# Kernel tuning notes

Hardware: AMD Instinct MI355X
Metric: run time of the kernel (lower is better)

Reference implementation:

```python
import jax, jax.numpy as jnp
import numpy as np

EPS = 1e-5

def binarize(w):
    # sign() binarization with straight-through estimator (identity grad)
    s = jnp.where(w >= 0, 1.0, -1.0).astype(w.dtype)
    return w + jax.lax.stop_gradient(s - w)

def batchnorm(x, gamma, beta):
    # BatchNorm1d in training mode: biased batch statistics over axis 0
    mean = jnp.mean(x, axis=0)
    var = jnp.mean(jnp.square(x - mean), axis=0)
    return (x - mean) * jax.lax.rsqrt(var + EPS) * gamma + beta

def setup_inputs() -> dict:
    key = jax.random.key(0)
    ks = jax.random.split(key, 3)
    B, D_IN, D_H, D_OUT = 65536, 784, 300, 10
    x = jax.random.normal(ks[0], (B, D_IN), dtype=jnp.float32)
    W1 = jax.random.normal(ks[1], (D_H, D_IN), dtype=jnp.float32) * 0.05
    W2 = jax.random.normal(ks[2], (D_OUT, D_H), dtype=jnp.float32) * 0.05
    gamma1 = jnp.ones((D_H,), jnp.float32)
    beta1 = jnp.zeros((D_H,), jnp.float32)
    gamma2 = jnp.ones((D_OUT,), jnp.float32)
    beta2 = jnp.zeros((D_OUT,), jnp.float32)
    return {"x": x, "W1": W1, "gamma1": gamma1, "beta1": beta1,
            "W2": W2, "gamma2": gamma2, "beta2": beta2}

def reference(x, W1, gamma1, beta1, W2, gamma2, beta2):
    h = x @ binarize(W1).T            # [B, 300]
    h = batchnorm(h, gamma1, beta1)
    o = h @ binarize(W2).T            # [B, 10]
    return batchnorm(o, gamma2, beta2)
```

## Files before the change

### kernel.cpp

```cpp
#include <hip/hip_runtime.h>
#include <cstdint>
#include <cstddef>

#define B_ROWS 65536
#define D_IN   784
#define KP     800
#define D_H    300
#define NP     320
#define D_OUT  10
#define NP2    16
#define EPS    1e-5f
#define NBLK   1024
#define APAD   44

typedef _Float16 half8  __attribute__((ext_vector_type(8)));
typedef float    floatx4 __attribute__((ext_vector_type(4)));

#define OFF_S1   ((size_t)0)
#define OFF_H    ((size_t)512000)
#define OFF_ST1  (OFF_H + (size_t)41943040)
#define OFF_W2   (OFF_ST1 + (size_t)2560)
#define OFF_ST2  (OFF_W2 + (size_t)10240)
#define OFF_OC   (OFF_ST2 + (size_t)256)
#define OFF_P1   OFF_OC
#define OFF_P2   (OFF_OC + (size_t)4194304)

__global__ void k_prep1(const float* __restrict__ W1, _Float16* __restrict__ S1)
{
    int idx = blockIdx.x * 256 + threadIdx.x;
    int n = idx / KP;
    int k = idx - n * KP;
    float v = 0.0f;
    if (n < D_H && k < D_IN)
        v = (W1[n * D_IN + k] >= 0.0f) ? 1.0f : -1.0f;
    S1[idx] = (_Float16)v;
}


#define PF_B(BV, NK)                                                        \
    _Pragma("unroll")                                                       \
    for (int nt = 0; nt < 5; ++nt)                                          \
        BV[nt] = *(const half8*)(bb + (size_t)nt * 16 * KP + (NK));

#define STAGE_LOAD(KK)                                                      \
    {                                                                       \
        sv0 = (floatx4){}; sv1 = (floatx4){};                               \
        if ((KK) + sc < D_IN) {               \
            sv0 = *(const floatx4*)(sxp + (KK));                            \
            sv1 = *(const floatx4*)(sxp + (KK) + 4);                        \
        }                                                                   \
    }

#define STAGE_STORE(BUF)                                                    \
    {                                                                       \
        half8 hv;                                                           \
        _Pragma("unroll")                                                   \
        for (int i2 = 0; i2 < 4; ++i2) {                                    \
            hv[i2]     = (_Float16)sv0[i2];                                 \
            hv[4 + i2] = (_Float16)sv1[i2];                                 \
        }                                                                   \
        *(half8*)&Alds[BUF][srow][sc] = hv;                                 \
    }

#define AFRAG(BUF)                                                          \
    _Pragma("unroll")                                                       \
    for (int mt = 0; mt < 4; ++mt)                                          \
        a[mt] = *(const half8*)&Alds[BUF][mt * 16 + row15][quad * 8];

#define COMPUTE(BV)                                                         \
    _Pragma("unroll")                                                       \
    for (int nt = 0; nt < 5; ++nt)                                          \
        _Pragma("unroll")                                                   \
        for (int mt = 0; mt < 4; ++mt)                                      \
            acc[mt][nt] = __builtin_amdgcn_mfma_f32_16x16x32_f16(           \
                a[mt], BV[nt], acc[mt][nt], 0, 0, 0);

__global__ __launch_bounds__(256) void k_gemm1(const float* __restrict__ x,
                                               const _Float16* __restrict__ S1,
                                               _Float16* __restrict__ h,
                                               float* __restrict__ part)
{
    __shared__ _Float16 Alds[2][64][APAD];
    const int t     = threadIdx.x;
    const int wave  = t >> 6;
    const int lane  = t & 63;
    const int row15 = lane & 15;
    const int quad  = lane >> 4;
    const int m0    = blockIdx.x * 64;

    const int srow = t >> 2;
    const int sc   = (t & 3) * 8;
    const float* sxp = x + (size_t)(m0 + srow) * D_IN + sc;

    const _Float16* bb = S1 + (size_t)(wave * 80 + row15) * KP + quad * 8;

    floatx4 acc[4][5] = {};
    half8   b0[5], b1[5];
    half8   a[4];
    floatx4 sv0, sv1;

    STAGE_LOAD(0)
    STAGE_STORE(0)
    PF_B(b0, 0)
    __syncthreads();

    for (int i = 0; i < 12; ++i) {
        const int kk = i * 64;
        STAGE_LOAD(kk + 32)
        PF_B(b1, kk + 32)
        AFRAG(0)
        COMPUTE(b0)
        STAGE_STORE(1)
        __syncthreads();
        STAGE_LOAD(kk + 64)
        PF_B(b0, kk + 64)
        AFRAG(1)
        COMPUTE(b1)
        STAGE_STORE(0)
        __syncthreads();
    }
    AFRAG(0)
    COMPUTE(b0)

    float s[5] = {}, q[5] = {};
#pragma unroll
    for (int mt = 0; mt < 4; ++mt)
#pragma unroll
        for (int nt = 0; nt < 5; ++nt)
#pragma unroll
            for (int r = 0; r < 4; ++r) {
                float v = acc[mt][nt][r];
                int m = m0 + mt * 16 + quad * 4 + r;
                int n = wave * 80 + nt * 16 + row15;
                h[(size_t)m * NP + n] = (_Float16)v;
                s[nt] += v;
                q[nt] += v * v;
            }
#pragma unroll
    for (int nt = 0; nt < 5; ++nt) {
        s[nt] += __shfl_xor(s[nt], 16); s[nt] += __shfl_xor(s[nt], 32);
        q[nt] += __shfl_xor(q[nt], 16); q[nt] += __shfl_xor(q[nt], 32);
    }
    if (quad == 0) {
#pragma unroll
        for (int nt = 0; nt < 5; ++nt) {
            int col = wave * 80 + nt * 16 + row15;
            part[(size_t)col * NBLK + blockIdx.x]        = s[nt];
            part[(size_t)(NP + col) * NBLK + blockIdx.x] = q[nt];
        }
    }
}

__global__ void k_stat1(const float* __restrict__ part, const float* __restrict__ gamma1,
                        const float* __restrict__ W2, _Float16* __restrict__ w2h)
{
    __shared__ float redS[4], redQ[4];
    const int j = blockIdx.x;
    const int t = threadIdx.x;
    const float* ps = part + (size_t)j * NBLK;
    const float* pq = part + (size_t)(NP + j) * NBLK;
    float s = ps[t] + ps[t + 256] + ps[t + 512] + ps[t + 768];
    float q = pq[t] + pq[t + 256] + pq[t + 512] + pq[t + 768];
#pragma unroll
    for (int off = 1; off < 64; off <<= 1) {
        s += __shfl_xor(s, off);
        q += __shfl_xor(q, off);
    }
    if ((t & 63) == 0) { redS[t >> 6] = s; redQ[t >> 6] = q; }
    __syncthreads();
    if (t < NP2) {
        float S = redS[0] + redS[1] + redS[2] + redS[3];
        float Q = redQ[0] + redQ[1] + redQ[2] + redQ[3];
        float mean = S * (1.0f / 65536.0f);
        float var  = Q * (1.0f / 65536.0f) - mean * mean;
        float a1   = 0.0f;
        if (j < D_H) a1 = gamma1[j] / sqrtf(var + EPS);
        float w = 0.0f;
        if (t < D_OUT && j < D_H)
            w = (W2[t * D_H + j] >= 0.0f) ? a1 : -a1;
        w2h[t * NP + j] = (_Float16)w;
    }
}

__global__ __launch_bounds__(256) void k_gemm2(const _Float16* __restrict__ h,
                                               const _Float16* __restrict__ w2h,
                                               float* __restrict__ oc,
                                               float* __restrict__ part2)
{
    __shared__ _Float16 Wlds[16][328];
    __shared__ float reds[4][16], redq[4][16];
    const int t     = threadIdx.x;
    const int wave  = t >> 6;
    const int lane  = t & 63;
    const int row15 = lane & 15;
    const int quad  = lane >> 4;

    for (int c = t; c < 640; c += 256) {
        int r  = c / 40;
        int cc = (c - r * 40) * 8;
        *(half8*)&Wlds[r][cc] = *(const half8*)(w2h + r * NP + cc);
    }
    __syncthreads();

    const int m0 = blockIdx.x * 64 + wave * 16;
    const _Float16* hp = h + (size_t)(m0 + row15) * NP + quad * 8;
    floatx4 acc = {};
#pragma unroll
    for (int kk = 0; kk < NP; kk += 32) {
        half8 a2 = *(const half8*)(hp + kk);
        half8 b2 = *(const half8*)&Wlds[row15][kk + quad * 8];
        acc = __builtin_amdgcn_mfma_f32_16x16x32_f16(a2, b2, acc, 0, 0, 0);
    }
    float s = 0.f, q = 0.f;
#pragma unroll
    for (int r = 0; r < 4; ++r) {
        float v = acc[r];
        oc[(size_t)(m0 + quad * 4 + r) * NP2 + row15] = v;
        s += v; q += v * v;
    }
    s += __shfl_xor(s, 16); s += __shfl_xor(s, 32);
    q += __shfl_xor(q, 16); q += __shfl_xor(q, 32);
    if (lane < 16) { reds[wave][row15] = s; redq[wave][row15] = q; }
    __syncthreads();
    if (t < 16) {
        float S = reds[0][t] + reds[1][t] + reds[2][t] + reds[3][t];
        float Q = redq[0][t] + redq[1][t] + redq[2][t] + redq[3][t];
        part2[(size_t)t * NBLK + blockIdx.x]          = S;
        part2[(size_t)(16 + t) * NBLK + blockIdx.x]   = Q;
    }
}

__global__ void k_stat2(const float* __restrict__ part2, const float* __restrict__ gamma2,
                        float* __restrict__ st2)
{
    __shared__ float redS[4], redQ[4];
    const int k = blockIdx.x;
    const int t = threadIdx.x;
    const float* ps = part2 + (size_t)k * NBLK;
    const float* pq = part2 + (size_t)(16 + k) * NBLK;
    float s = ps[t] + ps[t + 256] + ps[t + 512] + ps[t + 768];
    float q = pq[t] + pq[t + 256] + pq[t + 512] + pq[t + 768];
#pragma unroll
    for (int off = 1; off < 64; off <<= 1) {
        s += __shfl_xor(s, off);
        q += __shfl_xor(q, off);
    }
    if ((t & 63) == 0) { redS[t >> 6] = s; redQ[t >> 6] = q; }
    __syncthreads();
    if (t == 0) {
        float S = redS[0] + redS[1] + redS[2] + redS[3];
        float Q = redQ[0] + redQ[1] + redQ[2] + redQ[3];
        float mean = S * (1.0f / 65536.0f);
        float var  = Q * (1.0f / 65536.0f) - mean * mean;
        float sc   = (k < D_OUT) ? gamma2[k] / sqrtf(var + EPS) : 0.0f;
        st2[k]      = mean;
        st2[16 + k] = sc;
    }
}

__global__ void k_final(const float* __restrict__ oc, const float* __restrict__ st2,
                        const float* __restrict__ beta2, float* __restrict__ out)
{
    int idx = blockIdx.x * 256 + threadIdx.x;
    int m = idx / 10;
    int k = idx - m * 10;
    float mean = st2[k];
    float sc   = st2[16 + k];
    out[idx] = (oc[(size_t)m * NP2 + k] - mean) * sc + beta2[k];
}

extern "C" void kernel_launch(void* const* d_in, const int* in_sizes, int n_in,
                              void* d_out, int out_size, void* d_ws, size_t ws_size,
                              hipStream_t stream)
{
    const float* x      = (const float*)d_in[0];
    const float* W1     = (const float*)d_in[1];
    const float* gamma1 = (const float*)d_in[2];
    const float* W2     = (const float*)d_in[4];
    const float* gamma2 = (const float*)d_in[5];
    const float* beta2  = (const float*)d_in[6];
    float* out = (float*)d_out;

    char* ws = (char*)d_ws;
    _Float16* S1    = (_Float16*)(ws + OFF_S1);
    _Float16* h     = (_Float16*)(ws + OFF_H);
    _Float16* w2h   = (_Float16*)(ws + OFF_W2);
    float*    st2   = (float*)(ws + OFF_ST2);
    float*    oc    = (float*)(ws + OFF_OC);
    float*    part  = (float*)(ws + OFF_P1);
    float*    part2 = (float*)(ws + OFF_P2);

    k_prep1 <<<1000, 256, 0, stream>>>(W1, S1);
    k_gemm1 <<<NBLK, 256, 0, stream>>>(x, S1, h, part);
    k_stat1 <<<320, 256, 0, stream>>>(part, gamma1, W2, w2h);
    k_gemm2 <<<NBLK, 256, 0, stream>>>(h, w2h, oc, part2);
    k_stat2 <<<16, 256, 0, stream>>>(part2, gamma2, st2);
    k_final <<<2560, 256, 0, stream>>>(oc, st2, beta2, out);
}
```

Before: 103.9 us.

## Deepen A-tile prefetch and split MFMA phases with priority and sched barriers

The first GEMM kernel now keeps two register sets of staged x data, issuing global loads one extra K-step ahead so their latency overlaps more MFMA work. Each K-step's MFMA block is split into two halves, with the LDS fragment reads and stores interleaved between them, using explicit lgkmcnt waits and sched_barriers to fix instruction order. MFMA sections are raised with s_setprio. The aim is to hide global-load and LDS latency better, at the cost of more registers and hand-pinned scheduling that could limit the compiler.

```diff
diff --git a/kernel.cpp b/kernel.cpp
--- a/kernel.cpp
+++ b/kernel.cpp
@@ -42,38 +42,49 @@
     for (int nt = 0; nt < 5; ++nt)                                          \
         BV[nt] = *(const half8*)(bb + (size_t)nt * 16 * KP + (NK));
 
-#define STAGE_LOAD(KK)                                                      \
+#define STAGE_LOAD(V0, V1, KK)                                              \
     {                                                                       \
-        sv0 = (floatx4){}; sv1 = (floatx4){};                               \
+        V0 = (floatx4){}; V1 = (floatx4){};                                 \
         if ((KK) + sc < D_IN) {               \
-            sv0 = *(const floatx4*)(sxp + (KK));                            \
-            sv1 = *(const floatx4*)(sxp + (KK) + 4);                        \
+            V0 = *(const floatx4*)(sxp + (KK));                             \
+            V1 = *(const floatx4*)(sxp + (KK) + 4);                         \
         }                                                                   \
     }
 
-#define STAGE_STORE(BUF)                                                    \
+#define STAGE_STORE(V0, V1, BUF)                                            \
     {                                                                       \
         half8 hv;                                                           \
         _Pragma("unroll")                                                   \
         for (int i2 = 0; i2 < 4; ++i2) {                                    \
-            hv[i2]     = (_Float16)sv0[i2];                                 \
-            hv[4 + i2] = (_Float16)sv1[i2];                                 \
+            hv[i2]     = (_Float16)V0[i2];                                  \
+            hv[4 + i2] = (_Float16)V1[i2];                                  \
         }                                                                   \
         *(half8*)&Alds[BUF][srow][sc] = hv;                                 \
     }
 
-#define AFRAG(BUF)                                                          \
+#define AFRAG_H(BUF, H)                                                     \
     _Pragma("unroll")                                                       \
-    for (int mt = 0; mt < 4; ++mt)                                          \
+    for (int mt = 2 * (H); mt < 2 * (H) + 2; ++mt)                          \
         a[mt] = *(const half8*)&Alds[BUF][mt * 16 + row15][quad * 8];
 
-#define COMPUTE(BV)                                                         \
+#define COMPUTE_H(BV, H)                                                    \
+    __builtin_amdgcn_s_setprio(1);                                          \
     _Pragma("unroll")                                                       \
     for (int nt = 0; nt < 5; ++nt)                                          \
         _Pragma("unroll")                                                   \
-        for (int mt = 0; mt < 4; ++mt)                                      \
+        for (int mt = 2 * (H); mt < 2 * (H) + 2; ++mt)                      \
             acc[mt][nt] = __builtin_amdgcn_mfma_f32_16x16x32_f16(           \
-                a[mt], BV[nt], acc[mt][nt], 0, 0, 0);
+                a[mt], BV[nt], acc[mt][nt], 0, 0, 0);                       \
+    __builtin_amdgcn_s_setprio(0);
+
+#define LGKM0()                                                             \
+    asm volatile("s_waitcnt lgkmcnt(0)" ::: "memory");                      \
+    __builtin_amdgcn_sched_barrier(0);
+
+#define BARRIER()                                                           \
+    __builtin_amdgcn_sched_barrier(0);                                      \
+    __builtin_amdgcn_s_barrier();                                           \
+    __builtin_amdgcn_sched_barrier(0);
 
 __global__ __launch_bounds__(256) void k_gemm1(const float* __restrict__ x,
                                                const _Float16* __restrict__ S1,
@@ -97,30 +108,44 @@
     floatx4 acc[4][5] = {};
     half8   b0[5], b1[5];
     half8   a[4];
-    floatx4 sv0, sv1;
-
-    STAGE_LOAD(0)
-    STAGE_STORE(0)
+    floatx4 a0, a1, c0, c1;
+
+    STAGE_LOAD(a0, a1, 0)
     PF_B(b0, 0)
-    __syncthreads();
+    STAGE_LOAD(c0, c1, 32)
+    STAGE_STORE(a0, a1, 0)
+    LGKM0()
+    BARRIER()
 
     for (int i = 0; i < 12; ++i) {
         const int kk = i * 64;
-        STAGE_LOAD(kk + 32)
+        AFRAG_H(0, 0)
+        STAGE_LOAD(a0, a1, kk + 64)
+        LGKM0()
+        COMPUTE_H(b0, 0)
+        AFRAG_H(0, 1)
         PF_B(b1, kk + 32)
-        AFRAG(0)
-        COMPUTE(b0)
-        STAGE_STORE(1)
-        __syncthreads();
-        STAGE_LOAD(kk + 64)
+        STAGE_STORE(c0, c1, 1)
+        LGKM0()
+        COMPUTE_H(b0, 1)
+        BARRIER()
+        AFRAG_H(1, 0)
+        STAGE_LOAD(c0, c1, kk + 96)
+        LGKM0()
+        COMPUTE_H(b1, 0)
+        AFRAG_H(1, 1)
         PF_B(b0, kk + 64)
-        AFRAG(1)
-        COMPUTE(b1)
-        STAGE_STORE(0)
-        __syncthreads();
-    }
-    AFRAG(0)
-    COMPUTE(b0)
+        STAGE_STORE(a0, a1, 0)
+        LGKM0()
+        COMPUTE_H(b1, 1)
+        BARRIER()
+    }
+    AFRAG_H(0, 0)
+    LGKM0()
+    COMPUTE_H(b0, 0)
+    AFRAG_H(0, 1)
+    LGKM0()
+    COMPUTE_H(b0, 1)
 
     float s[5] = {}, q[5] = {};
 #pragma unroll
```

After: 110.4 us. 1.06x slower.

## Stage x tiles via direct global-to-LDS loads with swizzled fp32 layout

Applied to the files above, without the earlier changes.

Replaces the register-staged load, fp16 convert and LDS store of the x tile in the first GEMM with global_load_lds asynchronous copies of raw fp32 data into a XOR-swizzled LDS buffer. The fp16 conversion moves to fragment read time, and synchronization uses an explicit vmcnt wait plus s_barrier. The K tail is handled by pointing out-of-range lanes at a zeroed scratch buffer written by the prep kernel. This aims to cut VGPR pressure and instruction overhead in the load path, at the cost of doubling LDS footprint and repeating the conversion per fragment read.

```diff
diff --git a/kernel.cpp b/kernel.cpp
--- a/kernel.cpp
+++ b/kernel.cpp
@@ -11,22 +11,23 @@
 #define NP2    16
 #define EPS    1e-5f
 #define NBLK   1024
-#define APAD   44
 
 typedef _Float16 half8  __attribute__((ext_vector_type(8)));
 typedef float    floatx4 __attribute__((ext_vector_type(4)));
 
 #define OFF_S1   ((size_t)0)
 #define OFF_H    ((size_t)512000)
-#define OFF_ST1  (OFF_H + (size_t)41943040)
-#define OFF_W2   (OFF_ST1 + (size_t)2560)
+#define OFF_ZB   (OFF_H + (size_t)41943040)
+#define OFF_W2   (OFF_ZB + (size_t)2560)
 #define OFF_ST2  (OFF_W2 + (size_t)10240)
 #define OFF_OC   (OFF_ST2 + (size_t)256)
 #define OFF_P1   OFF_OC
 #define OFF_P2   (OFF_OC + (size_t)4194304)
 
-__global__ void k_prep1(const float* __restrict__ W1, _Float16* __restrict__ S1)
-{
+__global__ void k_prep1(const float* __restrict__ W1, _Float16* __restrict__ S1,
+                        float* __restrict__ zb)
+{
+    if (blockIdx.x == 0 && threadIdx.x < 16) zb[threadIdx.x] = 0.0f;
     int idx = blockIdx.x * 256 + threadIdx.x;
     int n = idx / KP;
     int k = idx - n * KP;
@@ -37,35 +38,40 @@
 }
 
 
+typedef const __attribute__((address_space(1))) void* gas_p;
+typedef __attribute__((address_space(3))) void* las_p;
+
+__device__ __forceinline__ void gload_lds16(const float* g, float* l)
+{
+    __builtin_amdgcn_global_load_lds((gas_p)g, (las_p)l, 16, 0, 0);
+}
+
 #define PF_B(BV, NK)                                                        \
     _Pragma("unroll")                                                       \
     for (int nt = 0; nt < 5; ++nt)                                          \
         BV[nt] = *(const half8*)(bb + (size_t)nt * 16 * KP + (NK));
 
-#define STAGE_LOAD(KK)                                                      \
-    {                                                                       \
-        sv0 = (floatx4){}; sv1 = (floatx4){};                               \
-        if ((KK) + sc < D_IN) {               \
-            sv0 = *(const floatx4*)(sxp + (KK));                            \
-            sv1 = *(const floatx4*)(sxp + (KK) + 4);                        \
-        }                                                                   \
-    }
-
-#define STAGE_STORE(BUF)                                                    \
-    {                                                                       \
+#define ISSUE_A(BUF, KK)                                                    \
+    gload_lds16(gA0 + (KK), &Afl[BUF][0][0] + lof);                         \
+    gload_lds16(gA1 + (KK), &Afl[BUF][0][0] + 1024 + lof);
+
+#define ISSUE_A_TAIL(BUF)                                                   \
+    gload_lds16(ts0, &Afl[BUF][0][0] + lof);                                \
+    gload_lds16(ts1, &Afl[BUF][0][0] + 1024 + lof);
+
+#define AFRAGF(BUF)                                                         \
+    _Pragma("unroll")                                                       \
+    for (int mt = 0; mt < 4; ++mt) {                                        \
+        floatx4 f0 = *(const floatx4*)&Afl[BUF][mt * 16 + row15][ce * 4];   \
+        floatx4 f1 = *(const floatx4*)&Afl[BUF][mt * 16 + row15][co * 4];   \
         half8 hv;                                                           \
         _Pragma("unroll")                                                   \
-        for (int i2 = 0; i2 < 4; ++i2) {                                    \
-            hv[i2]     = (_Float16)sv0[i2];                                 \
-            hv[4 + i2] = (_Float16)sv1[i2];                                 \
+        for (int j = 0; j < 4; ++j) {                                       \
+            hv[j]     = (_Float16)f0[j];                                    \
+            hv[4 + j] = (_Float16)f1[j];                                    \
         }                                                                   \
-        *(half8*)&Alds[BUF][srow][sc] = hv;                                 \
-    }
-
-#define AFRAG(BUF)                                                          \
-    _Pragma("unroll")                                                       \
-    for (int mt = 0; mt < 4; ++mt)                                          \
-        a[mt] = *(const half8*)&Alds[BUF][mt * 16 + row15][quad * 8];
+        a[mt] = hv;                                                         \
+    }
 
 #define COMPUTE(BV)                                                         \
     _Pragma("unroll")                                                       \
@@ -75,12 +81,20 @@
             acc[mt][nt] = __builtin_amdgcn_mfma_f32_16x16x32_f16(           \
                 a[mt], BV[nt], acc[mt][nt], 0, 0, 0);
 
+#define STEP_SYNC()                                                         \
+    __builtin_amdgcn_sched_barrier(0);                                      \
+    asm volatile("s_waitcnt vmcnt(5)" ::: "memory");                        \
+    __builtin_amdgcn_sched_barrier(0);                                      \
+    __builtin_amdgcn_s_barrier();                                           \
+    __builtin_amdgcn_sched_barrier(0);
+
 __global__ __launch_bounds__(256) void k_gemm1(const float* __restrict__ x,
                                                const _Float16* __restrict__ S1,
                                                _Float16* __restrict__ h,
-                                               float* __restrict__ part)
-{
-    __shared__ _Float16 Alds[2][64][APAD];
+                                               float* __restrict__ part,
+                                               const float* __restrict__ zb)
+{
+    __shared__ __align__(16) float Afl[2][64][32];
     const int t     = threadIdx.x;
     const int wave  = t >> 6;
     const int lane  = t & 63;
@@ -88,38 +102,44 @@
     const int quad  = lane >> 4;
     const int m0    = blockIdx.x * 64;
 
-    const int srow = t >> 2;
-    const int sc   = (t & 3) * 8;
-    const float* sxp = x + (size_t)(m0 + srow) * D_IN + sc;
+    const int rA   = wave * 8 + (lane >> 3);
+    const int cswz = (lane & 7) ^ ((lane >> 3) & 7);
+    const int lof  = wave * 256;
+    const float* gA0 = x + (size_t)(m0 + rA) * D_IN + cswz * 4;
+    const float* gA1 = gA0 + (size_t)32 * D_IN;
+    const float* ts0 = (cswz >= 4) ? zb : (gA0 + 768);
+    const float* ts1 = (cswz >= 4) ? zb : (gA1 + 768);
+
+    const int ce = (2 * quad) ^ (row15 & 7);
+    const int co = ce ^ 1;
 
     const _Float16* bb = S1 + (size_t)(wave * 80 + row15) * KP + quad * 8;
 
     floatx4 acc[4][5] = {};
     half8   b0[5], b1[5];
     half8   a[4];
-    floatx4 sv0, sv1;
-
-    STAGE_LOAD(0)
-    STAGE_STORE(0)
+
+    ISSUE_A(0, 0)
+    __builtin_amdgcn_sched_barrier(0);
     PF_B(b0, 0)
-    __syncthreads();
+    STEP_SYNC()
 
     for (int i = 0; i < 12; ++i) {
         const int kk = i * 64;
-        STAGE_LOAD(kk + 32)
+        ISSUE_A(1, kk + 32)
+        __builtin_amdgcn_sched_barrier(0);
         PF_B(b1, kk + 32)
-        AFRAG(0)
+        AFRAGF(0)
         COMPUTE(b0)
-        STAGE_STORE(1)
-        __syncthreads();
-        STAGE_LOAD(kk + 64)
+        STEP_SYNC()
+        if (i < 11) { ISSUE_A(0, kk + 64) } else { ISSUE_A_TAIL(0) }
+        __builtin_amdgcn_sched_barrier(0);
         PF_B(b0, kk + 64)
-        AFRAG(1)
+        AFRAGF(1)
         COMPUTE(b1)
-        STAGE_STORE(0)
-        __syncthreads();
-    }
-    AFRAG(0)
+        STEP_SYNC()
+    }
+    AFRAGF(0)
     COMPUTE(b0)
 
     float s[5] = {}, q[5] = {};
@@ -284,14 +304,15 @@
     char* ws = (char*)d_ws;
     _Float16* S1    = (_Float16*)(ws + OFF_S1);
     _Float16* h     = (_Float16*)(ws + OFF_H);
+    float*    zb    = (float*)(ws + OFF_ZB);
     _Float16* w2h   = (_Float16*)(ws + OFF_W2);
     float*    st2   = (float*)(ws + OFF_ST2);
     float*    oc    = (float*)(ws + OFF_OC);
     float*    part  = (float*)(ws + OFF_P1);
     float*    part2 = (float*)(ws + OFF_P2);
 
-    k_prep1 <<<1000, 256, 0, stream>>>(W1, S1);
-    k_gemm1 <<<NBLK, 256, 0, stream>>>(x, S1, h, part);
+    k_prep1 <<<1000, 256, 0, stream>>>(W1, S1, zb);
+    k_gemm1 <<<NBLK, 256, 0, stream>>>(x, S1, h, part, zb);
     k_stat1 <<<320, 256, 0, stream>>>(part, gamma1, W2, w2h);
     k_gemm2 <<<NBLK, 256, 0, stream>>>(h, w2h, oc, part2);
     k_stat2 <<<16, 256, 0, stream>>>(part2, gamma2, st2);
```

Result: faster. 91.79 us, median of 3 (-11.7%).
